# Kernel tuning notes

Measured on AMD Instinct MI355X. Metric: run time of the kernel, lower is better.

The kernel has to match this reference:

```python
import jax, jax.numpy as jnp
import numpy as np

B, L, S, N, D, DT, V, H = 32, 256, 5, 1024, 256, 256, 512, 8
Dh = D // H


def layernorm(x, g, b, eps=1e-5):
    m = x.mean(-1, keepdims=True)
    v = ((x - m) ** 2).mean(-1, keepdims=True)
    return (x - m) / jnp.sqrt(v + eps) * g + b


def setup_inputs() -> dict:
    key = jax.random.key(0)
    ks = jax.random.split(key, 16)
    sc = lambda k, shape: jax.random.normal(k, shape, jnp.float32) * 0.02
    return {
        'vis_tokens': jax.random.normal(ks[0], (B, N, D), jnp.float32),
        'left_ctx_ids': jax.random.randint(ks[1], (B, L, S), 0, V),
        'right_ctx_ids': jax.random.randint(ks[2], (B, L, S), 0, V),
        'tgt_ids': jax.random.randint(ks[3], (B, L), 0, V),
        'tgt_mask': jnp.ones((B, L), jnp.float32),
        'vis_mask': jax.random.uniform(ks[4], (B, L, N), jnp.float32),
        'emb_w': sc(ks[5], (V, DT)),          # tied embedding / classifier weight
        'dir_left': sc(ks[6], (DT,)),
        'dir_right': sc(ks[7], (DT,)),
        'txt_proj_w': sc(ks[8], (D, DT)), 'txt_proj_b': jnp.zeros((D,), jnp.float32),
        'q_gamma': jnp.ones((D,), jnp.float32), 'q_beta': jnp.zeros((D,), jnp.float32),
        'k_w': sc(ks[9], (D, D)), 'k_b': jnp.zeros((D,), jnp.float32),
        'v_w': sc(ks[10], (D, D)), 'v_b': jnp.zeros((D,), jnp.float32),
        'kv_gamma': jnp.ones((D,), jnp.float32), 'kv_beta': jnp.zeros((D,), jnp.float32),
        'tau': jnp.asarray(1.0, jnp.float32),
        'cls_b': jnp.zeros((V,), jnp.float32),
        'conv_w_l': sc(ks[11], (DT, DT, 3)),   # fresh random conv weight per call in torch
        'conv_w_r': sc(ks[12], (DT, DT, 3)),
    }


def _ctx_to_query(ctx_ids, dir_tok, conv_w, emb_w, txt_proj_w, txt_proj_b, qg, qb):
    E = emb_w[ctx_ids]                                    # [B,L,S,DT]
    q = jnp.transpose(E, (0, 1, 3, 2)).reshape(B * L, DT, S)
    q = jax.lax.conv_general_dilated(q, conv_w, (1,), [(1, 1)],
                                     dimension_numbers=('NCH', 'OIH', 'NCH'))  # [B*L,DT,S]
    # faithful to torch: flat reinterpretation [B*L,DT,S] -> [B,L,S,DT], then mean over dim 2
    q = q.reshape(B, L, -1, DT).mean(2)                   # [B,L,DT]
    q = q + dir_tok
    return layernorm(q @ txt_proj_w.T + txt_proj_b, qg, qb)  # [B,L,D]


def _cross_attend(Q, Fv, vis_mask, k_w, k_b, v_w, v_b, kvg, kvb, tau):
    K = layernorm(Fv @ k_w.T + k_b, kvg, kvb)             # [B,N,D]
    Vv = layernorm(Fv @ v_w.T + v_b, kvg, kvb)
    q = Q.reshape(B, L, H, Dh).transpose(0, 2, 1, 3)      # [B,H,L,Dh]
    k = K.reshape(B, N, H, Dh).transpose(0, 2, 1, 3)
    v = Vv.reshape(B, N, H, Dh).transpose(0, 2, 1, 3)
    tau_c = jnp.clip(tau, 0.25, 4.0)
    scores = jnp.einsum('bhld,bhnd->bhln', q, k) / (Dh ** 0.5 * tau_c)
    scores = scores * vis_mask[:, None]                   # multiplicative mask
    attn = jax.nn.softmax(scores, axis=-1)                # dropout = identity (eval)
    out = jnp.einsum('bhln,bhnd->bhld', attn, v)
    return out.transpose(0, 2, 1, 3).reshape(B, L, D)


def reference(vis_tokens, left_ctx_ids, right_ctx_ids, tgt_ids, tgt_mask, vis_mask,
              emb_w, dir_left, dir_right, txt_proj_w, txt_proj_b, q_gamma, q_beta,
              k_w, k_b, v_w, v_b, kv_gamma, kv_beta, tau, cls_b, conv_w_l, conv_w_r):
    Ql = _ctx_to_query(left_ctx_ids, dir_left, conv_w_l, emb_w, txt_proj_w, txt_proj_b, q_gamma, q_beta)
    Qr = _ctx_to_query(right_ctx_ids, dir_right, conv_w_r, emb_w, txt_proj_w, txt_proj_b, q_gamma, q_beta)
    Fl = _cross_attend(Ql, vis_tokens, vis_mask, k_w, k_b, v_w, v_b, kv_gamma, kv_beta, tau)
    Fr = _cross_attend(Qr, vis_tokens, vis_mask, k_w, k_b, v_w, v_b, kv_gamma, kv_beta, tau)
    logits_l = Fl @ emb_w.T + cls_b                       # tied classifier
    logits_r = Fr @ emb_w.T + cls_b
    p_l = jax.nn.softmax(logits_l / 2.0, axis=-1)
    p_r = jax.nn.softmax(logits_r / 2.0, axis=-1)
    agree = ((p_l[:, :-1, :] - p_r[:, 1:, :]) ** 2).sum(-1)
    denom = jnp.maximum(tgt_mask[:, :-1].sum(), 1.0)
    loss_sgm = 0.1 * (agree * tgt_mask[:, :-1]).sum() / denom
    return loss_sgm, logits_l, logits_r
```

## Files before the change

### kernel.cpp

```cpp
#include <hip/hip_runtime.h>

typedef __attribute__((ext_vector_type(8))) short short8;
typedef __attribute__((ext_vector_type(4))) short short4v;
typedef __attribute__((ext_vector_type(4))) float f32x4;

__device__ __forceinline__ short f2bf(float x) {
    union { float f; unsigned u; } c; c.f = x;
    unsigned u = c.u;
    u += 0x7fffu + ((u >> 16) & 1u);
    return (short)(u >> 16);
}

__global__ __launch_bounds__(256) void cvt_bf16(const float* __restrict__ s, short* __restrict__ d, int n4) {
    int i = blockIdx.x * 256 + threadIdx.x;
    if (i < n4) {
        float4 v = ((const float4*)s)[i];
        short4 o;
        o.x = f2bf(v.x); o.y = f2bf(v.y); o.z = f2bf(v.z); o.w = f2bf(v.w);
        ((short4*)d)[i] = o;
    }
}

__global__ __launch_bounds__(256) void cvt3(const float* __restrict__ emb, const float* __restrict__ kw,
                                            const float* __restrict__ vw,
                                            short* __restrict__ de, short* __restrict__ dk, short* __restrict__ dv) {
    int i = blockIdx.x * 256 + threadIdx.x;
    const float* s; short* d; int off;
    if (i < 32768) { s = emb; d = de; off = i; }
    else if (i < 49152) { s = kw; d = dk; off = i - 32768; }
    else { s = vw; d = dv; off = i - 49152; }
    float4 v = ((const float4*)s)[off];
    short4 o;
    o.x = f2bf(v.x); o.y = f2bf(v.y); o.z = f2bf(v.z); o.w = f2bf(v.w);
    ((short4*)d)[off] = o;
}

__global__ void build_wfold(const float* __restrict__ cl, const float* __restrict__ cr,
                            float* __restrict__ wfT) {
    const float* conv_w = blockIdx.y ? cr : cl;
    float* o = wfT + (long)blockIdx.y * 327680;
    const int ci = blockIdx.x;
    const int j = threadIdx.x;
    float acc[5] = {0.f, 0.f, 0.f, 0.f, 0.f};
#pragma unroll
    for (int i = 0; i < 5; ++i) {
        int flat = i * 256 + j;
        int c = flat / 5;
        int s = flat % 5;
#pragma unroll
        for (int k = 0; k < 3; ++k) {
            int si = s + k - 1;
            if (si >= 0 && si < 5) acc[si] += conv_w[(c * 256 + ci) * 3 + k];
        }
    }
#pragma unroll
    for (int si = 0; si < 5; ++si)
        o[(si * 256 + ci) * 256 + j] = acc[si] * 0.2f;
}

template <bool BIAS>
__global__ __launch_bounds__(256) void gemm64(const float* __restrict__ A,
                                              const float* __restrict__ W,
                                              const float* __restrict__ bias,
                                              float* __restrict__ C,
                                              int K, int ldC,
                                              long sliceA, long sliceW, long sliceC) {
    A += (long)blockIdx.z * sliceA;
    W += (long)blockIdx.z * sliceW;
    C += (long)blockIdx.z * sliceC;
    const int row0 = blockIdx.x * 64;
    const int col0 = blockIdx.y * 64;
    __shared__ float As[32][68];
    __shared__ float Ws[32][68];
    const int t = threadIdx.x;
    const int tx = t & 15;
    const int ty = t >> 4;
    float acc[4][4] = {};
    for (int kk = 0; kk < K; kk += 32) {
#pragma unroll
        for (int e = 0; e < 8; ++e) {
            int f = t + 256 * e;
            int r = f >> 5, kc = f & 31;
            As[kc][r] = A[(long)(row0 + r) * K + kk + kc];
            Ws[kc][r] = W[(long)(col0 + r) * K + kk + kc];
        }
        __syncthreads();
#pragma unroll
        for (int kc = 0; kc < 32; ++kc) {
            float4 a4 = *(const float4*)&As[kc][ty * 4];
            float4 w4 = *(const float4*)&Ws[kc][tx * 4];
            float av[4] = {a4.x, a4.y, a4.z, a4.w};
            float wv[4] = {w4.x, w4.y, w4.z, w4.w};
#pragma unroll
            for (int i = 0; i < 4; ++i)
#pragma unroll
                for (int jj = 0; jj < 4; ++jj)
                    acc[i][jj] += av[i] * wv[jj];
        }
        __syncthreads();
    }
#pragma unroll
    for (int r = 0; r < 4; ++r) {
        int row = row0 + ty * 4 + r;
#pragma unroll
        for (int c = 0; c < 4; ++c) {
            int col = col0 + tx * 4 + c;
            float v = acc[r][c];
            if (BIAS) v += bias[col];
            C[(long)row * ldC + col] = v;
        }
    }
}

__global__ __launch_bounds__(256) void gemm_bf(const short* __restrict__ A,
                                               const short* __restrict__ W,
                                               const float* __restrict__ bias,
                                               float* __restrict__ Cf,
                                               int K, int ldC,
                                               long sliceA, long sliceC) {
    A += (long)blockIdx.z * sliceA;
    const int row0 = blockIdx.x * 64, col0 = blockIdx.y * 64;
    __shared__ short As[64 * 40];
    __shared__ short Ws[64 * 40];
    const int t = threadIdx.x;
    const int wid = t >> 6, lane = t & 63, sub = lane & 15, quad = lane >> 4;
    const int wy = wid >> 1, wx = wid & 1;
    const int srow = t >> 2, sseg = t & 3;
    f32x4 acc00 = {0.f, 0.f, 0.f, 0.f}, acc01 = acc00, acc10 = acc00, acc11 = acc00;
    for (int kk = 0; kk < K; kk += 32) {
        *(short8*)&As[srow * 40 + sseg * 8] = *(const short8*)&A[(long)(row0 + srow) * K + kk + sseg * 8];
        *(short8*)&Ws[srow * 40 + sseg * 8] = *(const short8*)&W[(long)(col0 + srow) * K + kk + sseg * 8];
        __syncthreads();
        short8 a0 = *(const short8*)&As[(wy * 32 + sub) * 40 + quad * 8];
        short8 a1 = *(const short8*)&As[(wy * 32 + 16 + sub) * 40 + quad * 8];
        short8 b0 = *(const short8*)&Ws[(wx * 32 + sub) * 40 + quad * 8];
        short8 b1 = *(const short8*)&Ws[(wx * 32 + 16 + sub) * 40 + quad * 8];
        acc00 = __builtin_amdgcn_mfma_f32_16x16x32_bf16(a0, b0, acc00, 0, 0, 0);
        acc01 = __builtin_amdgcn_mfma_f32_16x16x32_bf16(a0, b1, acc01, 0, 0, 0);
        acc10 = __builtin_amdgcn_mfma_f32_16x16x32_bf16(a1, b0, acc10, 0, 0, 0);
        acc11 = __builtin_amdgcn_mfma_f32_16x16x32_bf16(a1, b1, acc11, 0, 0, 0);
        __syncthreads();
    }
    Cf += (long)blockIdx.z * sliceC;
#pragma unroll
    for (int i = 0; i < 2; ++i)
#pragma unroll
        for (int j = 0; j < 2; ++j) {
            f32x4 a = (i == 0) ? (j == 0 ? acc00 : acc01) : (j == 0 ? acc10 : acc11);
#pragma unroll
            for (int r = 0; r < 4; ++r) {
                int row = row0 + wy * 32 + i * 16 + quad * 4 + r;
                int col = col0 + wx * 32 + j * 16 + sub;
                Cf[(long)row * ldC + col] = a[r] + bias[col];
            }
        }
}

__global__ __launch_bounds__(256) void gemm_ln(const short* __restrict__ A,
                                               const short* __restrict__ kwbf, const short* __restrict__ vwbf,
                                               const float* __restrict__ k_b, const float* __restrict__ v_b,
                                               const float* __restrict__ gamma, const float* __restrict__ beta,
                                               short* __restrict__ Kout, short* __restrict__ Vt) {
    const bool isV = blockIdx.y != 0;
    const short* W = isV ? vwbf : kwbf;
    const float* bias = isV ? v_b : k_b;
    const int row0 = blockIdx.x * 64;
    __shared__ short As[64 * 40];
    __shared__ short Ws[256 * 40];
    __shared__ float s_mu[64 * 4];
    __shared__ float s_sq[64 * 4];
    __shared__ float s_mv[64 * 2];
    const int t = threadIdx.x;
    const int wid = t >> 6, lane = t & 63, sub = lane & 15, quad = lane >> 4;
    f32x4 acc[4][4];
#pragma unroll
    for (int mi = 0; mi < 4; ++mi)
#pragma unroll
        for (int ni = 0; ni < 4; ++ni) acc[mi][ni] = (f32x4){0.f, 0.f, 0.f, 0.f};

    const int sr = t >> 2, sseg = t & 3;
    for (int kk = 0; kk < 256; kk += 32) {
        *(short8*)&As[sr * 40 + sseg * 8] = *(const short8*)&A[(long)(row0 + sr) * 256 + kk + sseg * 8];
#pragma unroll
        for (int i = 0; i < 4; ++i) {
            int r = i * 64 + sr;
            *(short8*)&Ws[r * 40 + sseg * 8] = *(const short8*)&W[(long)r * 256 + kk + sseg * 8];
        }
        __syncthreads();
        short8 a[4], b[4];
#pragma unroll
        for (int mi = 0; mi < 4; ++mi) a[mi] = *(const short8*)&As[(mi * 16 + sub) * 40 + quad * 8];
#pragma unroll
        for (int ni = 0; ni < 4; ++ni) b[ni] = *(const short8*)&Ws[(wid * 64 + ni * 16 + sub) * 40 + quad * 8];
#pragma unroll
        for (int mi = 0; mi < 4; ++mi)
#pragma unroll
            for (int ni = 0; ni < 4; ++ni)
                acc[mi][ni] = __builtin_amdgcn_mfma_f32_16x16x32_bf16(a[mi], b[ni], acc[mi][ni], 0, 0, 0);
        __syncthreads();
    }
#pragma unroll
    for (int ni = 0; ni < 4; ++ni) {
        float bv = bias[wid * 64 + ni * 16 + sub];
#pragma unroll
        for (int mi = 0; mi < 4; ++mi)
#pragma unroll
            for (int r = 0; r < 4; ++r) acc[mi][ni][r] += bv;
    }
#pragma unroll
    for (int mi = 0; mi < 4; ++mi) {
#pragma unroll
        for (int r = 0; r < 4; ++r) {
            float s = 0.f, q2 = 0.f;
#pragma unroll
            for (int ni = 0; ni < 4; ++ni) {
                float v = acc[mi][ni][r];
                s += v; q2 += v * v;
            }
#pragma unroll
            for (int off = 8; off; off >>= 1) {
                s += __shfl_xor(s, off, 16);
                q2 += __shfl_xor(q2, off, 16);
            }
            if (sub == 0) {
                int row = mi * 16 + quad * 4 + r;
                s_mu[row * 4 + wid] = s;
                s_sq[row * 4 + wid] = q2;
            }
        }
    }
    __syncthreads();
    if (t < 64) {
        float s = s_mu[t * 4] + s_mu[t * 4 + 1] + s_mu[t * 4 + 2] + s_mu[t * 4 + 3];
        float q2 = s_sq[t * 4] + s_sq[t * 4 + 1] + s_sq[t * 4 + 2] + s_sq[t * 4 + 3];
        float mean = s * (1.0f / 256.0f);
        float var = q2 * (1.0f / 256.0f) - mean * mean;
        s_mv[t * 2] = mean;
        s_mv[t * 2 + 1] = rsqrtf(var + 1e-5f);
    }
    __syncthreads();
#pragma unroll
    for (int ni = 0; ni < 4; ++ni) {
        int col = wid * 64 + ni * 16 + sub;
        float g = gamma[col], bb = beta[col];
        if (!isV) {
#pragma unroll
            for (int mi = 0; mi < 4; ++mi)
#pragma unroll
                for (int r = 0; r < 4; ++r) {
                    int row = mi * 16 + quad * 4 + r;
                    float v = (acc[mi][ni][r] - s_mv[row * 2]) * s_mv[row * 2 + 1] * g + bb;
                    Kout[(long)(row0 + row) * 256 + col] = f2bf(v);
                }
        } else {
            int h = col >> 5, dh = col & 31;
#pragma unroll
            for (int mi = 0; mi < 4; ++mi) {
                int rowb = row0 + mi * 16 + quad * 4;
                short4 o;
#pragma unroll
                for (int r = 0; r < 4; ++r) {
                    int row = mi * 16 + quad * 4 + r;
                    float v = (acc[mi][ni][r] - s_mv[row * 2]) * s_mv[row * 2 + 1] * g + bb;
                    ((short*)&o)[r] = f2bf(v);
                }
                int gb = rowb >> 10, n = rowb & 1023;
                *(short4*)&Vt[((long)(gb * 8 + h) * 32 + dh) * 1024 + n] = o;
            }
        }
    }
}

__global__ __launch_bounds__(256) void bias_dir_kernel(const float* __restrict__ tp, const float* __restrict__ tpb,
                                                       const float* __restrict__ dirL, const float* __restrict__ dirR,
                                                       float* __restrict__ biasL, float* __restrict__ biasR) {
    const float* dir = blockIdx.y ? dirR : dirL;
    float* outp = blockIdx.y ? biasR : biasL;
    __shared__ float sdir[256];
    sdir[threadIdx.x] = dir[threadIdx.x];
    __syncthreads();
    const int wid = threadIdx.x >> 6, lane = threadIdx.x & 63;
#pragma unroll
    for (int i = 0; i < 8; ++i) {
        const int d = blockIdx.x * 32 + wid * 8 + i;
        float p = 0.f;
#pragma unroll
        for (int jj = 0; jj < 4; ++jj)
            p += tp[d * 256 + jj * 64 + lane] * sdir[jj * 64 + lane];
#pragma unroll
        for (int off = 32; off; off >>= 1) p += __shfl_xor(p, off, 64);
        if (lane == 0) outp[d] = p + tpb[d];
    }
}

__global__ __launch_bounds__(256) void q_build(const int* __restrict__ idsL, const int* __restrict__ idsR,
                                               const float* __restrict__ Pp,
                                               const float* __restrict__ biasL, const float* __restrict__ biasR,
                                               const float* __restrict__ qg, const float* __restrict__ qb,
                                               short* __restrict__ Qbf) {
    const int wid = threadIdx.x >> 6, lane = threadIdx.x & 63;
    const int bl = blockIdx.x * 4 + wid;
    const bool right = blockIdx.y != 0;
    const int* ids = right ? idsR : idsL;
    const float* P = right ? Pp + 655360 : Pp;
    const float* bias = right ? biasR : biasL;
    const int d0 = lane * 4;
    float4 acc = *(const float4*)&bias[d0];
#pragma unroll
    for (int s = 0; s < 5; ++s) {
        int tok = ids[bl * 5 + s];
        float4 p = *(const float4*)&P[(long)(s * 512 + tok) * 256 + d0];
        acc.x += p.x; acc.y += p.y; acc.z += p.z; acc.w += p.w;
    }
    float sum = acc.x + acc.y + acc.z + acc.w;
    float sq = acc.x * acc.x + acc.y * acc.y + acc.z * acc.z + acc.w * acc.w;
#pragma unroll
    for (int off = 32; off; off >>= 1) {
        sum += __shfl_xor(sum, off, 64);
        sq += __shfl_xor(sq, off, 64);
    }
    float mean = sum * (1.0f / 256.0f);
    float var = sq * (1.0f / 256.0f) - mean * mean;
    float rstd = rsqrtf(var + 1e-5f);
    float4 g = *(const float4*)&qg[d0];
    float4 bb = *(const float4*)&qb[d0];
    short4 o;
    o.x = f2bf((acc.x - mean) * rstd * g.x + bb.x);
    o.y = f2bf((acc.y - mean) * rstd * g.y + bb.y);
    o.z = f2bf((acc.z - mean) * rstd * g.z + bb.z);
    o.w = f2bf((acc.w - mean) * rstd * g.w + bb.w);
    *(short4*)&Qbf[(right ? 2097152L : 0L) + (long)bl * 256 + d0] = o;
}

__device__ __forceinline__ void proc_chunk(
    short8 ak0, short8 ak1, short4v v00, short4v v01, short4v v10, short4v v11,
    const float* mlds, int sub, int quad, float inv2,
    const short8 (&bqL)[4], const short8 (&bqR)[4],
    f32x4 (&oL)[4][2], f32x4 (&oR)[4][2], float (&psL)[4], float (&psR)[4]) {
    short8 av0, av1;
#pragma unroll
    for (int j = 0; j < 4; ++j) {
        av0[j] = v00[j]; av0[4 + j] = v01[j];
        av1[j] = v10[j]; av1[4 + j] = v11[j];
    }
    const int sw = (quad ^ (sub & 7)) << 2;
#pragma unroll
    for (int lt = 0; lt < 4; ++lt) {
        const int mi = ((lt * 16 + sub) << 5) + sw;
        float4 mk0 = *(const float4*)&mlds[mi];
        float4 mk1 = *(const float4*)&mlds[mi ^ 16];
        float m0x = mk0.x * inv2, m0y = mk0.y * inv2, m0z = mk0.z * inv2, m0w = mk0.w * inv2;
        float m1x = mk1.x * inv2, m1y = mk1.y * inv2, m1z = mk1.z * inv2, m1w = mk1.w * inv2;
        {
            f32x4 c0 = {0.f, 0.f, 0.f, 0.f}, c1 = c0;
            c0 = __builtin_amdgcn_mfma_f32_16x16x32_bf16(ak0, bqL[lt], c0, 0, 0, 0);
            c1 = __builtin_amdgcn_mfma_f32_16x16x32_bf16(ak1, bqL[lt], c1, 0, 0, 0);
            float p0 = __builtin_amdgcn_exp2f(c0[0] * m0x);
            float p1 = __builtin_amdgcn_exp2f(c0[1] * m0y);
            float p2 = __builtin_amdgcn_exp2f(c0[2] * m0z);
            float p3 = __builtin_amdgcn_exp2f(c0[3] * m0w);
            float p4 = __builtin_amdgcn_exp2f(c1[0] * m1x);
            float p5 = __builtin_amdgcn_exp2f(c1[1] * m1y);
            float p6 = __builtin_amdgcn_exp2f(c1[2] * m1z);
            float p7 = __builtin_amdgcn_exp2f(c1[3] * m1w);
            psL[lt] += ((p0 + p1) + (p2 + p3)) + ((p4 + p5) + (p6 + p7));
            short8 p8;
            p8[0] = f2bf(p0); p8[1] = f2bf(p1); p8[2] = f2bf(p2); p8[3] = f2bf(p3);
            p8[4] = f2bf(p4); p8[5] = f2bf(p5); p8[6] = f2bf(p6); p8[7] = f2bf(p7);
            oL[lt][0] = __builtin_amdgcn_mfma_f32_16x16x32_bf16(av0, p8, oL[lt][0], 0, 0, 0);
            oL[lt][1] = __builtin_amdgcn_mfma_f32_16x16x32_bf16(av1, p8, oL[lt][1], 0, 0, 0);
        }
        {
            f32x4 c0 = {0.f, 0.f, 0.f, 0.f}, c1 = c0;
            c0 = __builtin_amdgcn_mfma_f32_16x16x32_bf16(ak0, bqR[lt], c0, 0, 0, 0);
            c1 = __builtin_amdgcn_mfma_f32_16x16x32_bf16(ak1, bqR[lt], c1, 0, 0, 0);
            float p0 = __builtin_amdgcn_exp2f(c0[0] * m0x);
            float p1 = __builtin_amdgcn_exp2f(c0[1] * m0y);
            float p2 = __builtin_amdgcn_exp2f(c0[2] * m0z);
            float p3 = __builtin_amdgcn_exp2f(c0[3] * m0w);
            float p4 = __builtin_amdgcn_exp2f(c1[0] * m1x);
            float p5 = __builtin_amdgcn_exp2f(c1[1] * m1y);
            float p6 = __builtin_amdgcn_exp2f(c1[2] * m1z);
            float p7 = __builtin_amdgcn_exp2f(c1[3] * m1w);
            psR[lt] += ((p0 + p1) + (p2 + p3)) + ((p4 + p5) + (p6 + p7));
            short8 p8;
            p8[0] = f2bf(p0); p8[1] = f2bf(p1); p8[2] = f2bf(p2); p8[3] = f2bf(p3);
            p8[4] = f2bf(p4); p8[5] = f2bf(p5); p8[6] = f2bf(p6); p8[7] = f2bf(p7);
            oR[lt][0] = __builtin_amdgcn_mfma_f32_16x16x32_bf16(av0, p8, oR[lt][0], 0, 0, 0);
            oR[lt][1] = __builtin_amdgcn_mfma_f32_16x16x32_bf16(av1, p8, oR[lt][1], 0, 0, 0);
        }
    }
}

__global__ __launch_bounds__(512, 1) void attn_wave(const short* __restrict__ Qbf,
                                                    const short* __restrict__ Kbf,
                                                    const short* __restrict__ Vt,
                                                    const float* __restrict__ vis_mask,
                                                    const float* __restrict__ tau_p,
                                                    short* __restrict__ Fbf) {
    const int t = threadIdx.x;
    const int wid = t >> 6, lane = t & 63, sub = lane & 15, quad = lane >> 4;
    const int gb = ((blockIdx.x & 7) << 5) | (blockIdx.x >> 3);
    const int b = gb >> 3;
    const int lb = (gb >> 1) & 3;
    const int hq = gb & 1;
    const int wh = wid >> 1, nh = wid & 1;
    const int h = hq * 4 + wh;
    const int l0 = lb * 64;
    float tau = fminf(fmaxf(tau_p[0], 0.25f), 4.0f);
    const float inv2 = 1.4426950408889634f / (5.656854249492381f * tau);

    __shared__ float mbuf[2 * 4096];
    __shared__ float red[4][64][72];

    const int s0 = t * 2;
    const int l_s = (s0 >> 3) & 63, nh_s = s0 >> 9;
    const int n4a = s0 & 7, n4b = n4a + 1;
    const float* mrow0 = vis_mask + (long)(b * 256 + l0 + l_s) * 1024 + nh_s * 512 + 4 * (n4a ^ (l_s & 7));
    const float* mrow1 = vis_mask + (long)(b * 256 + l0 + l_s) * 1024 + nh_s * 512 + 4 * (n4b ^ (l_s & 7));
    float* mdst0 = mbuf + nh_s * 2048 + l_s * 32 + n4a * 4;
    float* mdst1 = mbuf + nh_s * 2048 + l_s * 32 + n4b * 4;

    short8 bqL[4], bqR[4];
#pragma unroll
    for (int lt = 0; lt < 4; ++lt) {
        const long qoff = (long)(b * 256 + l0 + lt * 16 + sub) * 256 + h * 32 + quad * 8;
        bqL[lt] = *(const short8*)&Qbf[qoff];
        bqR[lt] = *(const short8*)&Qbf[2097152 + qoff];
    }

    const short* Kb = Kbf + (long)b * 262144 + h * 32;
    const short* Vb = Vt + (long)(b * 8 + h) * 32768;
    const float* mld = mbuf + nh * 2048;

    f32x4 oL[4][2], oR[4][2];
    float psL[4], psR[4];
#pragma unroll
    for (int lt = 0; lt < 4; ++lt) {
        oL[lt][0] = (f32x4){0.f, 0.f, 0.f, 0.f}; oL[lt][1] = oL[lt][0];
        oR[lt][0] = oL[lt][0]; oR[lt][1] = oL[lt][0];
        psL[lt] = 0.f; psR[lt] = 0.f;
    }

    const int nbeg = nh << 9;

#define LOADK(A0, A1, N)                                                      \
    A0 = *(const short8*)&Kb[(long)((N) + sub) * 256 + quad * 8];             \
    A1 = *(const short8*)&Kb[(long)((N) + 16 + sub) * 256 + quad * 8];
#define LOADV(W00, W01, W10, W11, N)                                          \
    W00 = *(const short4v*)&Vb[(long)sub * 1024 + (N) + quad * 4];            \
    W01 = *(const short4v*)&Vb[(long)sub * 1024 + (N) + 16 + quad * 4];       \
    W10 = *(const short4v*)&Vb[(long)(16 + sub) * 1024 + (N) + quad * 4];     \
    W11 = *(const short4v*)&Vb[(long)(16 + sub) * 1024 + (N) + 16 + quad * 4];

    short8 ak0A, ak1A, ak0B, ak1B;
    short4v v00A, v01A, v10A, v11A, v00B, v01B, v10B, v11B;
    float4 mr0, mr1;

    mr0 = *(const float4*)&mrow0[0];
    mr1 = *(const float4*)&mrow1[0];
    *(float4*)&mdst0[0] = mr0;
    *(float4*)&mdst1[0] = mr1;
    LOADK(ak0A, ak1A, nbeg)
    LOADV(v00A, v01A, v10A, v11A, nbeg)
    __syncthreads();

#pragma unroll 1
    for (int j = 0; j < 8; ++j) {
        const int n0 = nbeg + j * 64;
        LOADK(ak0B, ak1B, n0 + 32)
        LOADV(v00B, v01B, v10B, v11B, n0 + 32)
        {
            const int nrel = j * 64 + 32;
            mr0 = *(const float4*)&mrow0[nrel];
            mr1 = *(const float4*)&mrow1[nrel];
        }
        proc_chunk(ak0A, ak1A, v00A, v01A, v10A, v11A, mld, sub, quad, inv2,
                   bqL, bqR, oL, oR, psL, psR);
        *(float4*)&mdst0[4096] = mr0;
        *(float4*)&mdst1[4096] = mr1;
        __syncthreads();
        const int nx = (j < 7) ? n0 + 64 : nbeg;
        LOADK(ak0A, ak1A, nx)
        LOADV(v00A, v01A, v10A, v11A, nx)
        {
            const int nrel = (j < 7) ? j * 64 + 64 : 0;
            mr0 = *(const float4*)&mrow0[nrel];
            mr1 = *(const float4*)&mrow1[nrel];
        }
        proc_chunk(ak0B, ak1B, v00B, v01B, v10B, v11B, mld + 4096, sub, quad, inv2,
                   bqL, bqR, oL, oR, psL, psR);
        *(float4*)&mdst0[0] = mr0;
        *(float4*)&mdst1[0] = mr1;
        __syncthreads();
    }
#undef LOADK
#undef LOADV

#pragma unroll
    for (int lt = 0; lt < 4; ++lt) {
        psL[lt] += __shfl_xor(psL[lt], 16, 64); psL[lt] += __shfl_xor(psL[lt], 32, 64);
        psR[lt] += __shfl_xor(psR[lt], 16, 64); psR[lt] += __shfl_xor(psR[lt], 32, 64);
    }

    if (nh == 1) {
        float* p = &red[wh][lane][0];
#pragma unroll
        for (int lt = 0; lt < 4; ++lt) {
            *(f32x4*)(p + lt * 8) = oL[lt][0];
            *(f32x4*)(p + lt * 8 + 4) = oL[lt][1];
            *(f32x4*)(p + 32 + lt * 8) = oR[lt][0];
            *(f32x4*)(p + 32 + lt * 8 + 4) = oR[lt][1];
            p[64 + lt] = psL[lt];
            p[68 + lt] = psR[lt];
        }
    }
    __syncthreads();
    if (nh == 1) return;
    {
        const float* p = &red[wh][lane][0];
#pragma unroll
        for (int lt = 0; lt < 4; ++lt) {
            f32x4 e0 = *(const f32x4*)(p + lt * 8);
            f32x4 e1 = *(const f32x4*)(p + lt * 8 + 4);
            f32x4 e2 = *(const f32x4*)(p + 32 + lt * 8);
            f32x4 e3 = *(const f32x4*)(p + 32 + lt * 8 + 4);
#pragma unroll
            for (int q = 0; q < 4; ++q) {
                oL[lt][0][q] += e0[q]; oL[lt][1][q] += e1[q];
                oR[lt][0][q] += e2[q]; oR[lt][1][q] += e3[q];
            }
            psL[lt] += p[64 + lt];
            psR[lt] += p[68 + lt];
        }
    }

#pragma unroll
    for (int lt = 0; lt < 4; ++lt) {
        const long fo = (long)(b * 256 + l0 + lt * 16 + sub) * 256 + h * 32 + quad * 4;
        const float rL = 1.0f / psL[lt], rR = 1.0f / psR[lt];
        short4v s0v, s1v;
#pragma unroll
        for (int r = 0; r < 4; ++r) { s0v[r] = f2bf(oL[lt][0][r] * rL); s1v[r] = f2bf(oL[lt][1][r] * rL); }
        *(short4v*)&Fbf[fo] = s0v;
        *(short4v*)&Fbf[fo + 16] = s1v;
#pragma unroll
        for (int r = 0; r < 4; ++r) { s0v[r] = f2bf(oR[lt][0][r] * rR); s1v[r] = f2bf(oR[lt][1][r] * rR); }
        *(short4v*)&Fbf[2097152 + fo] = s0v;
        *(short4v*)&Fbf[2097152 + fo + 16] = s1v;
    }
}

__global__ __launch_bounds__(256) void loss_pair(const float* __restrict__ logits,
                                                 const float* __restrict__ tgt_mask,
                                                 float* __restrict__ partials) {
    const int wid = threadIdx.x >> 6, lane = threadIdx.x & 63;
    const int pid = blockIdx.x * 4 + wid;
    const int b = pid / 255, l = pid - b * 255;
    const float* ll = logits + (long)(b * 256 + l) * 512;
    const float* lr = logits + 4194304 + (long)(b * 256 + l + 1) * 512;
    float a[8], c[8];
#pragma unroll
    for (int j = 0; j < 8; ++j) {
        a[j] = ll[lane + 64 * j] * 0.5f;
        c[j] = lr[lane + 64 * j] * 0.5f;
    }
    float ml = -1e30f, mr = -1e30f;
#pragma unroll
    for (int j = 0; j < 8; ++j) { ml = fmaxf(ml, a[j]); mr = fmaxf(mr, c[j]); }
#pragma unroll
    for (int off = 32; off; off >>= 1) {
        ml = fmaxf(ml, __shfl_xor(ml, off, 64));
        mr = fmaxf(mr, __shfl_xor(mr, off, 64));
    }
    float sl = 0.f, sr = 0.f;
#pragma unroll
    for (int j = 0; j < 8; ++j) {
        a[j] = __expf(a[j] - ml); sl += a[j];
        c[j] = __expf(c[j] - mr); sr += c[j];
    }
#pragma unroll
    for (int off = 32; off; off >>= 1) {
        sl += __shfl_xor(sl, off, 64);
        sr += __shfl_xor(sr, off, 64);
    }
    float rl = 1.0f / sl, rr = 1.0f / sr;
    float sq = 0.f;
#pragma unroll
    for (int j = 0; j < 8; ++j) {
        float d = a[j] * rl - c[j] * rr;
        sq += d * d;
    }
#pragma unroll
    for (int off = 32; off; off >>= 1) sq += __shfl_xor(sq, off, 64);

    __shared__ float sred[4];
    if (lane == 0) sred[wid] = sq * tgt_mask[b * 256 + l];
    __syncthreads();
    if (threadIdx.x == 0)
        partials[blockIdx.x] = (sred[0] + sred[1]) + (sred[2] + sred[3]);
}

__global__ __launch_bounds__(256) void loss_final(const float* __restrict__ tgt_mask,
                                                  const float* __restrict__ partials,
                                                  float* __restrict__ outp) {
    const int t = threadIdx.x;
    float s = 0.f, acc = 0.f;
    for (int i = t; i < 32 * 255; i += 256) {
        int b = i / 255, l = i % 255;
        s += tgt_mask[b * 256 + l];
    }
    for (int i = t; i < 2040; i += 256) acc += partials[i];
    __shared__ float red[256];
    __shared__ float reda[256];
    red[t] = s;
    reda[t] = acc;
    __syncthreads();
    for (int st = 128; st; st >>= 1) {
        if (t < st) { red[t] += red[t + st]; reda[t] += reda[t + st]; }
        __syncthreads();
    }
    if (t == 0) outp[0] = 0.1f * reda[0] / fmaxf(red[0], 1.0f);
}

extern "C" void kernel_launch(void* const* d_in, const int* in_sizes, int n_in,
                              void* d_out, int out_size, void* d_ws, size_t ws_size,
                              hipStream_t stream) {
    const float* vis_tokens = (const float*)d_in[0];
    const int* idsL = (const int*)d_in[1];
    const int* idsR = (const int*)d_in[2];
    const float* tgt_mask = (const float*)d_in[4];
    const float* vis_mask = (const float*)d_in[5];
    const float* emb_w = (const float*)d_in[6];
    const float* dirL = (const float*)d_in[7];
    const float* dirR = (const float*)d_in[8];
    const float* tp_w = (const float*)d_in[9];
    const float* tp_b = (const float*)d_in[10];
    const float* q_g = (const float*)d_in[11];
    const float* q_b = (const float*)d_in[12];
    const float* k_w = (const float*)d_in[13];
    const float* k_b = (const float*)d_in[14];
    const float* v_w = (const float*)d_in[15];
    const float* v_b = (const float*)d_in[16];
    const float* kv_g = (const float*)d_in[17];
    const float* kv_b = (const float*)d_in[18];
    const float* tau = (const float*)d_in[19];
    const float* cls_b = (const float*)d_in[20];
    const float* conv_l = (const float*)d_in[21];
    const float* conv_r = (const float*)d_in[22];
    float* out = (float*)d_out;

    short* sws = (short*)d_ws;
    short* visbf = sws;
    short* embbf = visbf + 8388608;
    short* kwbf  = embbf + 131072;
    short* vwbf  = kwbf + 65536;
    short* Kbf   = vwbf + 65536;
    short* Vt    = Kbf + 8388608;
    short* Qbf   = Vt + 8388608;
    short* Fbf   = Qbf + 4194304;
    float* wfT   = (float*)(Fbf + 4194304);
    float* Ms    = wfT + 655360;
    float* Pp    = Ms + 655360;
    float* bias_l = Pp + 1310720;
    float* bias_r = bias_l + 256;
    float* partials = bias_r + 256;

    cvt_bf16<<<8192, 256, 0, stream>>>(vis_tokens, visbf, 2097152);
    cvt3<<<256, 256, 0, stream>>>(emb_w, k_w, v_w, embbf, kwbf, vwbf);

    build_wfold<<<dim3(256, 2), 256, 0, stream>>>(conv_l, conv_r, wfT);
    gemm64<false><<<dim3(4, 4, 10), 256, 0, stream>>>(tp_w, wfT, nullptr, Ms, 256, 256, 0, 65536, 65536);
    gemm64<false><<<dim3(8, 4, 10), 256, 0, stream>>>(emb_w, Ms, nullptr, Pp, 256, 256, 0, 65536, 131072);
    bias_dir_kernel<<<dim3(8, 2), 256, 0, stream>>>(tp_w, tp_b, dirL, dirR, bias_l, bias_r);
    q_build<<<dim3(2048, 2), 256, 0, stream>>>(idsL, idsR, Pp, bias_l, bias_r, q_g, q_b, Qbf);

    gemm_ln<<<dim3(512, 2), 256, 0, stream>>>(visbf, kwbf, vwbf, k_b, v_b, kv_g, kv_b, Kbf, Vt);

    attn_wave<<<256, 512, 0, stream>>>(Qbf, Kbf, Vt, vis_mask, tau, Fbf);

    gemm_bf<<<dim3(128, 8, 2), 256, 0, stream>>>(Fbf, embbf, cls_b, out + 1, 256, 512,
                                                 2097152, 4194304);

    loss_pair<<<2040, 256, 0, stream>>>(out + 1, tgt_mask, partials);
    loss_final<<<1, 256, 0, stream>>>(tgt_mask, partials, out);
}
```

Before: 325.1 us.

## Split left/right attention sides across waves and double attention grid

Each wave in the attention kernel now handles only one side (left or right query) instead of both, with blocks covering two heads instead of four. The grid doubles to 512 blocks and launch bounds allow four blocks per CU, reducing per-wave register pressure so occupancy can rise. The trade-off is that each K/V chunk and mask tile is loaded by twice as many waves/blocks, increasing memory traffic, and the cross-wave reduction buffer shrinks.

Measured after the change: 407.8 us. 1.25x slower.

```diff
diff --git a/kernel.cpp b/kernel.cpp
--- a/kernel.cpp
+++ b/kernel.cpp
@@ -335,8 +335,8 @@
 __device__ __forceinline__ void proc_chunk(
     short8 ak0, short8 ak1, short4v v00, short4v v01, short4v v10, short4v v11,
     const float* mlds, int sub, int quad, float inv2,
-    const short8 (&bqL)[4], const short8 (&bqR)[4],
-    f32x4 (&oL)[4][2], f32x4 (&oR)[4][2], float (&psL)[4], float (&psR)[4]) {
+    const short8 (&bq)[4],
+    f32x4 (&o)[4][2], float (&ps)[4]) {
     short8 av0, av1;
 #pragma unroll
     for (int j = 0; j < 4; ++j) {
@@ -351,48 +351,27 @@
         float4 mk1 = *(const float4*)&mlds[mi ^ 16];
         float m0x = mk0.x * inv2, m0y = mk0.y * inv2, m0z = mk0.z * inv2, m0w = mk0.w * inv2;
         float m1x = mk1.x * inv2, m1y = mk1.y * inv2, m1z = mk1.z * inv2, m1w = mk1.w * inv2;
-        {
-            f32x4 c0 = {0.f, 0.f, 0.f, 0.f}, c1 = c0;
-            c0 = __builtin_amdgcn_mfma_f32_16x16x32_bf16(ak0, bqL[lt], c0, 0, 0, 0);
-            c1 = __builtin_amdgcn_mfma_f32_16x16x32_bf16(ak1, bqL[lt], c1, 0, 0, 0);
-            float p0 = __builtin_amdgcn_exp2f(c0[0] * m0x);
-            float p1 = __builtin_amdgcn_exp2f(c0[1] * m0y);
-            float p2 = __builtin_amdgcn_exp2f(c0[2] * m0z);
-            float p3 = __builtin_amdgcn_exp2f(c0[3] * m0w);
-            float p4 = __builtin_amdgcn_exp2f(c1[0] * m1x);
-            float p5 = __builtin_amdgcn_exp2f(c1[1] * m1y);
-            float p6 = __builtin_amdgcn_exp2f(c1[2] * m1z);
-            float p7 = __builtin_amdgcn_exp2f(c1[3] * m1w);
-            psL[lt] += ((p0 + p1) + (p2 + p3)) + ((p4 + p5) + (p6 + p7));
-            short8 p8;
-            p8[0] = f2bf(p0); p8[1] = f2bf(p1); p8[2] = f2bf(p2); p8[3] = f2bf(p3);
-            p8[4] = f2bf(p4); p8[5] = f2bf(p5); p8[6] = f2bf(p6); p8[7] = f2bf(p7);
-            oL[lt][0] = __builtin_amdgcn_mfma_f32_16x16x32_bf16(av0, p8, oL[lt][0], 0, 0, 0);
-            oL[lt][1] = __builtin_amdgcn_mfma_f32_16x16x32_bf16(av1, p8, oL[lt][1], 0, 0, 0);
-        }
-        {
-            f32x4 c0 = {0.f, 0.f, 0.f, 0.f}, c1 = c0;
-            c0 = __builtin_amdgcn_mfma_f32_16x16x32_bf16(ak0, bqR[lt], c0, 0, 0, 0);
-            c1 = __builtin_amdgcn_mfma_f32_16x16x32_bf16(ak1, bqR[lt], c1, 0, 0, 0);
-            float p0 = __builtin_amdgcn_exp2f(c0[0] * m0x);
-            float p1 = __builtin_amdgcn_exp2f(c0[1] * m0y);
-            float p2 = __builtin_amdgcn_exp2f(c0[2] * m0z);
-            float p3 = __builtin_amdgcn_exp2f(c0[3] * m0w);
-            float p4 = __builtin_amdgcn_exp2f(c1[0] * m1x);
-            float p5 = __builtin_amdgcn_exp2f(c1[1] * m1y);
-            float p6 = __builtin_amdgcn_exp2f(c1[2] * m1z);
-            float p7 = __builtin_amdgcn_exp2f(c1[3] * m1w);
-            psR[lt] += ((p0 + p1) + (p2 + p3)) + ((p4 + p5) + (p6 + p7));
-            short8 p8;
-            p8[0] = f2bf(p0); p8[1] = f2bf(p1); p8[2] = f2bf(p2); p8[3] = f2bf(p3);
-            p8[4] = f2bf(p4); p8[5] = f2bf(p5); p8[6] = f2bf(p6); p8[7] = f2bf(p7);
-            oR[lt][0] = __builtin_amdgcn_mfma_f32_16x16x32_bf16(av0, p8, oR[lt][0], 0, 0, 0);
-            oR[lt][1] = __builtin_amdgcn_mfma_f32_16x16x32_bf16(av1, p8, oR[lt][1], 0, 0, 0);
-        }
-    }
-}
-
-__global__ __launch_bounds__(512, 1) void attn_wave(const short* __restrict__ Qbf,
+        f32x4 c0 = {0.f, 0.f, 0.f, 0.f}, c1 = c0;
+        c0 = __builtin_amdgcn_mfma_f32_16x16x32_bf16(ak0, bq[lt], c0, 0, 0, 0);
+        c1 = __builtin_amdgcn_mfma_f32_16x16x32_bf16(ak1, bq[lt], c1, 0, 0, 0);
+        float p0 = __builtin_amdgcn_exp2f(c0[0] * m0x);
+        float p1 = __builtin_amdgcn_exp2f(c0[1] * m0y);
+        float p2 = __builtin_amdgcn_exp2f(c0[2] * m0z);
+        float p3 = __builtin_amdgcn_exp2f(c0[3] * m0w);
+        float p4 = __builtin_amdgcn_exp2f(c1[0] * m1x);
+        float p5 = __builtin_amdgcn_exp2f(c1[1] * m1y);
+        float p6 = __builtin_amdgcn_exp2f(c1[2] * m1z);
+        float p7 = __builtin_amdgcn_exp2f(c1[3] * m1w);
+        ps[lt] += ((p0 + p1) + (p2 + p3)) + ((p4 + p5) + (p6 + p7));
+        short8 p8;
+        p8[0] = f2bf(p0); p8[1] = f2bf(p1); p8[2] = f2bf(p2); p8[3] = f2bf(p3);
+        p8[4] = f2bf(p4); p8[5] = f2bf(p5); p8[6] = f2bf(p6); p8[7] = f2bf(p7);
+        o[lt][0] = __builtin_amdgcn_mfma_f32_16x16x32_bf16(av0, p8, o[lt][0], 0, 0, 0);
+        o[lt][1] = __builtin_amdgcn_mfma_f32_16x16x32_bf16(av1, p8, o[lt][1], 0, 0, 0);
+    }
+}
+
+__global__ __launch_bounds__(512, 4) void attn_wave(const short* __restrict__ Qbf,
                                                     const short* __restrict__ Kbf,
                                                     const short* __restrict__ Vt,
                                                     const float* __restrict__ vis_mask,
@@ -400,18 +379,20 @@
                                                     short* __restrict__ Fbf) {
     const int t = threadIdx.x;
     const int wid = t >> 6, lane = t & 63, sub = lane & 15, quad = lane >> 4;
-    const int gb = ((blockIdx.x & 7) << 5) | (blockIdx.x >> 3);
-    const int b = gb >> 3;
-    const int lb = (gb >> 1) & 3;
-    const int hq = gb & 1;
-    const int wh = wid >> 1, nh = wid & 1;
-    const int h = hq * 4 + wh;
+    const int gb = ((blockIdx.x & 7) << 6) | (blockIdx.x >> 3);
+    const int b = gb >> 4;
+    const int lb = (gb >> 2) & 3;
+    const int hp = gb & 3;
+    const int wh = wid >> 2;
+    const int side = (wid >> 1) & 1;
+    const int nh = wid & 1;
+    const int h = hp * 2 + wh;
     const int l0 = lb * 64;
     float tau = fminf(fmaxf(tau_p[0], 0.25f), 4.0f);
     const float inv2 = 1.4426950408889634f / (5.656854249492381f * tau);
 
     __shared__ float mbuf[2 * 4096];
-    __shared__ float red[4][64][72];
+    __shared__ float red[4][64][40];
 
     const int s0 = t * 2;
     const int l_s = (s0 >> 3) & 63, nh_s = s0 >> 9;
@@ -421,25 +402,24 @@
     float* mdst0 = mbuf + nh_s * 2048 + l_s * 32 + n4a * 4;
     float* mdst1 = mbuf + nh_s * 2048 + l_s * 32 + n4b * 4;
 
-    short8 bqL[4], bqR[4];
+    const short* Qside = Qbf + (side ? 2097152L : 0L);
+    short8 bq[4];
 #pragma unroll
     for (int lt = 0; lt < 4; ++lt) {
         const long qoff = (long)(b * 256 + l0 + lt * 16 + sub) * 256 + h * 32 + quad * 8;
-        bqL[lt] = *(const short8*)&Qbf[qoff];
-        bqR[lt] = *(const short8*)&Qbf[2097152 + qoff];
+        bq[lt] = *(const short8*)&Qside[qoff];
     }
 
     const short* Kb = Kbf + (long)b * 262144 + h * 32;
     const short* Vb = Vt + (long)(b * 8 + h) * 32768;
     const float* mld = mbuf + nh * 2048;
 
-    f32x4 oL[4][2], oR[4][2];
-    float psL[4], psR[4];
+    f32x4 o[4][2];
+    float ps[4];
 #pragma unroll
     for (int lt = 0; lt < 4; ++lt) {
-        oL[lt][0] = (f32x4){0.f, 0.f, 0.f, 0.f}; oL[lt][1] = oL[lt][0];
-        oR[lt][0] = oL[lt][0]; oR[lt][1] = oL[lt][0];
-        psL[lt] = 0.f; psR[lt] = 0.f;
+        o[lt][0] = (f32x4){0.f, 0.f, 0.f, 0.f}; o[lt][1] = o[lt][0];
+        ps[lt] = 0.f;
     }
 
     const int nbeg = nh << 9;
@@ -476,7 +456,7 @@
             mr1 = *(const float4*)&mrow1[nrel];
         }
         proc_chunk(ak0A, ak1A, v00A, v01A, v10A, v11A, mld, sub, quad, inv2,
-                   bqL, bqR, oL, oR, psL, psR);
+                   bq, o, ps);
         *(float4*)&mdst0[4096] = mr0;
         *(float4*)&mdst1[4096] = mr1;
         __syncthreads();
@@ -489,7 +469,7 @@
             mr1 = *(const float4*)&mrow1[nrel];
         }
         proc_chunk(ak0B, ak1B, v00B, v01B, v10B, v11B, mld + 4096, sub, quad, inv2,
-                   bqL, bqR, oL, oR, psL, psR);
+                   bq, o, ps);
         *(float4*)&mdst0[0] = mr0;
         *(float4*)&mdst1[0] = mr1;
         __syncthreads();
@@ -499,55 +479,47 @@
 
 #pragma unroll
     for (int lt = 0; lt < 4; ++lt) {
-        psL[lt] += __shfl_xor(psL[lt], 16, 64); psL[lt] += __shfl_xor(psL[lt], 32, 64);
-        psR[lt] += __shfl_xor(psR[lt], 16, 64); psR[lt] += __shfl_xor(psR[lt], 32, 64);
-    }
-
+        ps[lt] += __shfl_xor(ps[lt], 16, 64);
+        ps[lt] += __shfl_xor(ps[lt], 32, 64);
+    }
+
+    const int pr = wid >> 1;
     if (nh == 1) {
-        float* p = &red[wh][lane][0];
+        float* p = &red[pr][lane][0];
 #pragma unroll
         for (int lt = 0; lt < 4; ++lt) {
-            *(f32x4*)(p + lt * 8) = oL[lt][0];
-            *(f32x4*)(p + lt * 8 + 4) = oL[lt][1];
-            *(f32x4*)(p + 32 + lt * 8) = oR[lt][0];
-            *(f32x4*)(p + 32 + lt * 8 + 4) = oR[lt][1];
-            p[64 + lt] = psL[lt];
-            p[68 + lt] = psR[lt];
+            *(f32x4*)(p + lt * 8) = o[lt][0];
+            *(f32x4*)(p + lt * 8 + 4) = o[lt][1];
+            p[32 + lt] = ps[lt];
         }
     }
     __syncthreads();
     if (nh == 1) return;
     {
-        const float* p = &red[wh][lane][0];
+        const float* p = &red[pr][lane][0];
 #pragma unroll
         for (int lt = 0; lt < 4; ++lt) {
             f32x4 e0 = *(const f32x4*)(p + lt * 8);
             f32x4 e1 = *(const f32x4*)(p + lt * 8 + 4);
-            f32x4 e2 = *(const f32x4*)(p + 32 + lt * 8);
-            f32x4 e3 = *(const f32x4*)(p + 32 + lt * 8 + 4);
 #pragma unroll
             for (int q = 0; q < 4; ++q) {
-                oL[lt][0][q] += e0[q]; oL[lt][1][q] += e1[q];
-                oR[lt][0][q] += e2[q]; oR[lt][1][q] += e3[q];
+                o[lt][0][q] += e0[q];
+                o[lt][1][q] += e1[q];
             }
-            psL[lt] += p[64 + lt];
-            psR[lt] += p[68 + lt];
-        }
-    }
-
+            ps[lt] += p[32 + lt];
+        }
+    }
+
+    short* Fside = Fbf + (side ? 2097152L : 0L);
 #pragma unroll
     for (int lt = 0; lt < 4; ++lt) {
         const long fo = (long)(b * 256 + l0 + lt * 16 + sub) * 256 + h * 32 + quad * 4;
-        const float rL = 1.0f / psL[lt], rR = 1.0f / psR[lt];
+        const float rS = 1.0f / ps[lt];
         short4v s0v, s1v;
 #pragma unroll
-        for (int r = 0; r < 4; ++r) { s0v[r] = f2bf(oL[lt][0][r] * rL); s1v[r] = f2bf(oL[lt][1][r] * rL); }
-        *(short4v*)&Fbf[fo] = s0v;
-        *(short4v*)&Fbf[fo + 16] = s1v;
-#pragma unroll
-        for (int r = 0; r < 4; ++r) { s0v[r] = f2bf(oR[lt][0][r] * rR); s1v[r] = f2bf(oR[lt][1][r] * rR); }
-        *(short4v*)&Fbf[2097152 + fo] = s0v;
-        *(short4v*)&Fbf[2097152 + fo + 16] = s1v;
+        for (int r = 0; r < 4; ++r) { s0v[r] = f2bf(o[lt][0][r] * rS); s1v[r] = f2bf(o[lt][1][r] * rS); }
+        *(short4v*)&Fside[fo] = s0v;
+        *(short4v*)&Fside[fo + 16] = s1v;
     }
 }
 
@@ -677,7 +649,7 @@
 
     gemm_ln<<<dim3(512, 2), 256, 0, stream>>>(visbf, kwbf, vwbf, k_b, v_b, kv_g, kv_b, Kbf, Vt);
 
-    attn_wave<<<256, 512, 0, stream>>>(Qbf, Kbf, Vt, vis_mask, tau, Fbf);
+    attn_wave<<<512, 512, 0, stream>>>(Qbf, Kbf, Vt, vis_mask, tau, Fbf);
 
     gemm_bf<<<dim3(128, 8, 2), 256, 0, stream>>>(Fbf, embbf, cls_b, out + 1, 256, 512,
                                                  2097152, 4194304);
```
